# Optimization experiments

Hardware: AMD Instinct MI355X
Metric: run time of the kernel (lower is better)

The kernel has to match this reference:

```python
import jax, jax.numpy as jnp
import numpy as np

GAMMA = 0.7
WALK_LEN = 3
TAU = 1.0
N_FILTERS = 8


def _row_norm(A):
    return A / jnp.clip(jnp.sum(A, axis=-1, keepdims=True), 1e-12, None)


def _motif_channel(A, idx, Wadj, gates):
    # A: [n,n]; idx: [I,k] int node indices; Wadj: [F,k,k]; gates: [L]
    n = A.shape[0]
    I, k = idx.shape
    F = Wadj.shape[0]
    # learnable filter adjacency: softplus, symmetrize, zero diagonal, row-normalize
    S = jax.nn.softplus(Wadj)
    S = 0.5 * (S + jnp.swapaxes(S, -1, -2)) * (1.0 - jnp.eye(k, dtype=A.dtype))
    Sf = _row_norm(S)                                  # [F,k,k]
    # per-instance induced subgraph transition matrices
    As = A[idx[:, :, None], idx[:, None, :]]           # [I,k,k]
    Tm = _row_norm(As)                                 # [I,k,k]
    # batched Kronecker product: Km[i,f,a*k+b,c*k+d] = Tm[i,a,c]*Sf[f,b,d]
    Km = (Tm[:, None, :, None, :, None] * Sf[None, :, None, :, None, :]).reshape(I, F, k * k, k * k)
    gp = jax.nn.softplus(gates)                        # [L] length gates
    M = Km
    acc = (GAMMA * gp[0]) * jnp.trace(M, axis1=-2, axis2=-1)   # [I,F]
    for p in range(2, WALK_LEN + 1):
        M = M @ Km
        acc = acc + (GAMMA ** p * gp[p - 1]) * jnp.trace(M, axis1=-2, axis2=-1)
    sims = acc                                         # [I,F] RWK similarities
    alphas = jax.nn.softmax(sims / max(1e-06, TAU), axis=-1)
    contrib = (alphas * sims) / float(k)               # [I,F]
    upd = jnp.broadcast_to(contrib[:, None, :], (I, k, F)).reshape(I * k, F)
    return jnp.zeros((n, F), A.dtype).at[idx.reshape(-1)].add(upd)


def _layer(A, tri_idx, cyc_idx, H, Wt, Wc, g, lng, lnb, w1, b1, w2, b2):
    Phi = jnp.concatenate([_motif_channel(A, tri_idx, Wt, g),
                           _motif_channel(A, cyc_idx, Wc, g),
                           H], axis=1)                 # [n, in_ch]
    mu = jnp.mean(Phi, axis=-1, keepdims=True)
    var = jnp.var(Phi, axis=-1, keepdims=True)
    X = (Phi - mu) / jnp.sqrt(var + 1e-5) * lng + lnb  # LayerNorm
    return jax.nn.gelu(X @ w1 + b1, approximate=False) @ w2 + b2  # dropout = identity (eval)


def _templates():
    tri = np.zeros((3, 3), np.float32)
    for u, v in [(0, 1), (1, 2), (0, 2)]:
        tri[u, v] = tri[v, u] = 1.0
    cyc = np.zeros((4, 4), np.float32)
    for u, v in [(0, 1), (1, 2), (2, 3), (3, 0)]:
        cyc[u, v] = cyc[v, u] = 1.0
    return tri, cyc


def setup_inputs() -> dict:
    key = jax.random.key(0)
    ks = jax.random.split(key, 16)
    n, D, HID = 4096, 128, 128
    A = (jax.random.uniform(ks[0], (n, n)) < 0.01).astype(jnp.float32)
    A = 0.5 * (A + A.T)
    A = A * (1.0 - jnp.eye(n, dtype=jnp.float32))
    tri_idx = jax.random.randint(ks[1], (30000, 3), 0, n, dtype=jnp.int32)
    cyc_idx = jax.random.randint(ks[2], (15000, 4), 0, n, dtype=jnp.int32)
    tri_t, cyc_t = _templates()
    def w_adj(k, tmpl):
        return jnp.asarray(tmpl)[None] + 0.05 * jax.random.normal(k, (N_FILTERS,) + tmpl.shape, dtype=jnp.float32)
    in0, in1 = 17, 145
    inp = {"A_full": A, "tri_idx": tri_idx, "cyc_idx": cyc_idx,
           "W_tri_0": w_adj(ks[3], tri_t), "W_cyc_0": w_adj(ks[4], cyc_t),
           "gates_0": jnp.zeros((WALK_LEN,), jnp.float32),
           "lng_0": jnp.ones((in0,), jnp.float32), "lnb_0": jnp.zeros((in0,), jnp.float32),
           "w1_0": 0.05 * jax.random.normal(ks[5], (in0, HID), jnp.float32), "b1_0": jnp.zeros((HID,), jnp.float32),
           "w2_0": 0.05 * jax.random.normal(ks[6], (HID, D), jnp.float32), "b2_0": jnp.zeros((D,), jnp.float32),
           "W_tri_1": w_adj(ks[7], tri_t), "W_cyc_1": w_adj(ks[8], cyc_t),
           "gates_1": jnp.zeros((WALK_LEN,), jnp.float32),
           "lng_1": jnp.ones((in1,), jnp.float32), "lnb_1": jnp.zeros((in1,), jnp.float32),
           "w1_1": 0.05 * jax.random.normal(ks[9], (in1, HID), jnp.float32), "b1_1": jnp.zeros((HID,), jnp.float32),
           "w2_1": 0.05 * jax.random.normal(ks[10], (HID, D), jnp.float32), "b2_1": jnp.zeros((D,), jnp.float32)}
    return inp


def reference(A_full, tri_idx, cyc_idx,
              W_tri_0, W_cyc_0, gates_0, lng_0, lnb_0, w1_0, b1_0, w2_0, b2_0,
              W_tri_1, W_cyc_1, gates_1, lng_1, lnb_1, w1_1, b1_1, w2_1, b2_1):
    # base channel (use_base=True): node degree from dense adjacency
    H = jnp.sum(A_full, axis=-1, keepdims=True)        # [n,1]
    Z = _layer(A_full, tri_idx, cyc_idx, H, W_tri_0, W_cyc_0, gates_0, lng_0, lnb_0, w1_0, b1_0, w2_0, b2_0)
    H = jnp.concatenate([Z, H], axis=1)                # residual_cat: [n,129]
    Z = _layer(A_full, tri_idx, cyc_idx, H, W_tri_1, W_cyc_1, gates_1, lng_1, lnb_1, w1_1, b1_1, w2_1, b2_1)
    H = jnp.concatenate([Z, H], axis=1)                # [n,257]
    return H
```

## Files before the change

kernel.cpp:

```cpp
#include <hip/hip_runtime.h>
#include <math.h>
#include <stdint.h>

#define GAMMA 0.7f
#define CAP 96

typedef __attribute__((ext_vector_type(8))) short short8v;
typedef __attribute__((ext_vector_type(4))) float f32x4;

__device__ __forceinline__ float sp_dev(float x) {
    return fmaxf(x, 0.0f) + log1pf(expf(-fabsf(x)));
}
__device__ __forceinline__ float gelu_exact(float x) {
    return 0.5f * x * (1.0f + erff(x * 0.70710678118654752f));
}
__device__ __forceinline__ uint16_t f2bf(float x) {
    union { float f; uint32_t u; } c; c.f = x;
    uint32_t u = c.u + 0x7FFFu + ((c.u >> 16) & 1u);
    return (uint16_t)(u >> 16);
}

__global__ void prep_kernel(const float* __restrict__ Wt0, const float* __restrict__ Wc0,
                            const float* __restrict__ g0,
                            const float* __restrict__ Wt1, const float* __restrict__ Wc1,
                            const float* __restrict__ g1,
                            const float* __restrict__ w1_0, const float* __restrict__ w2_0,
                            const float* __restrict__ w1_1, const float* __restrict__ w2_1,
                            float* __restrict__ dcoef,
                            uint16_t* __restrict__ Wb10, uint16_t* __restrict__ Wb20,
                            uint16_t* __restrict__ Wb11, uint16_t* __restrict__ Wb21,
                            int* __restrict__ cursor, int ncur) {
    int tid = threadIdx.x;
    int gtid = blockIdx.x * blockDim.x + tid;
    int stride = gridDim.x * blockDim.x;

    for (int i = gtid; i < ncur; i += stride) cursor[i] = 0;

    if (blockIdx.x == 0 && tid < 32) {
        int L = tid >> 4, m = (tid >> 3) & 1, f = tid & 7;
        int k = m ? 4 : 3;
        const float* W = L ? (m ? Wc1 : Wt1) : (m ? Wc0 : Wt0);
        const float* g = L ? g1 : g0;
        float S[4][4], Y[4][4];
        for (int a = 0; a < k; a++)
            for (int b = 0; b < k; b++)
                S[a][b] = sp_dev(W[(f * k + a) * k + b]);
        for (int a = 0; a < k; a++)
            for (int b = 0; b < k; b++)
                Y[a][b] = (a == b) ? 0.0f : 0.5f * (S[a][b] + S[b][a]);
        for (int a = 0; a < k; a++) {
            float rs = 0.0f;
            for (int b = 0; b < k; b++) rs += Y[a][b];
            rs = fmaxf(rs, 1e-12f);
            for (int b = 0; b < k; b++) Y[a][b] /= rs;
        }
        float t1 = 0, t2 = 0, t3 = 0;
        for (int a = 0; a < k; a++) t1 += Y[a][a];
        for (int a = 0; a < k; a++)
            for (int b = 0; b < k; b++) t2 += Y[a][b] * Y[b][a];
        for (int a = 0; a < k; a++)
            for (int b = 0; b < k; b++)
                for (int c = 0; c < k; c++) t3 += Y[a][b] * Y[b][c] * Y[c][a];
        float* d = dcoef + ((L * 2 + m) * 8 + f) * 3;
        d[0] = GAMMA * sp_dev(g[0]) * t1;
        d[1] = GAMMA * GAMMA * sp_dev(g[1]) * t2;
        d[2] = GAMMA * GAMMA * GAMMA * sp_dev(g[2]) * t3;
    }
    for (int idx = gtid; idx < 57344; idx += stride) {
        if (idx < 4096) {
            int c = idx >> 5, k = idx & 31;
            Wb10[idx] = (k < 17) ? f2bf(w1_0[k * 128 + c]) : 0;
        } else if (idx < 20480) {
            int e = idx - 4096; int c = e >> 7, k = e & 127;
            Wb20[e] = f2bf(w2_0[k * 128 + c]);
        } else if (idx < 40960) {
            int e = idx - 20480; int c = e / 160, k = e % 160;
            Wb11[e] = (k < 145) ? f2bf(w1_1[k * 128 + c]) : 0;
        } else {
            int e = idx - 40960; int c = e >> 7, k = e & 127;
            Wb21[e] = f2bf(w2_1[k * 128 + c]);
        }
    }
}

template <int K>
__device__ __forceinline__ void contrib_group(
    const float* __restrict__ A, int n,
    const int* __restrict__ idx, int I, int i, int g, int lane,
    const float (*dc)[8][3], float* __restrict__ cont,
    int* __restrict__ cursor, int* __restrict__ slotbuf) {
    int base = lane & ~3;
    int mynode = (g < K) ? idx[i * K + g] : 0;
    int nb0 = __shfl(mynode, base + 0);
    int nb1 = __shfl(mynode, base + 1);
    int nb2 = __shfl(mynode, base + 2);
    int nb3 = (K == 4) ? __shfl(mynode, base + 3) : 0;

    float r0, r1, r2, r3;
    if (K == 3) {
        if (g < 3) {
            const float* Ar = A + (size_t)mynode * n;
            r0 = Ar[nb0]; r1 = Ar[nb1]; r2 = Ar[nb2]; r3 = 0.0f;
        } else {
            r0 = 0.0f; r1 = 0.0f; r2 = 0.0f; r3 = 1.0f;
        }
    } else {
        const float* Ar = A + (size_t)mynode * n;
        r0 = Ar[nb0]; r1 = Ar[nb1]; r2 = Ar[nb2]; r3 = Ar[nb3];
    }
    float rs = fmaxf(r0 + r1 + r2 + r3, 1e-12f);
    float inv = 1.0f / rs;
    r0 *= inv; r1 *= inv; r2 *= inv; r3 *= inv;

    float M[4][4];
#pragma unroll
    for (int b = 0; b < 4; b++) {
        M[b][0] = __shfl(r0, base + b);
        M[b][1] = __shfl(r1, base + b);
        M[b][2] = __shfl(r2, base + b);
        M[b][3] = __shfl(r3, base + b);
    }

    float t1 = M[0][0] + M[1][1] + M[2][2] + M[3][3];
    float t2 = 0.0f, t3 = 0.0f;
#pragma unroll
    for (int a = 0; a < 4; a++)
#pragma unroll
        for (int b = 0; b < 4; b++) {
            float ab = M[a][b];
            t2 += ab * M[b][a];
#pragma unroll
            for (int c = 0; c < 4; c++) t3 += ab * M[b][c] * M[c][a];
        }
    if (K == 3) { t1 -= 1.0f; t2 -= 1.0f; t3 -= 1.0f; }

#pragma unroll
    for (int L = 0; L < 2; L++) {
        float sims[8], mx = -1e30f;
#pragma unroll
        for (int f = 0; f < 8; f++) {
            sims[f] = dc[L][f][0] * t1 + dc[L][f][1] * t2 + dc[L][f][2] * t3;
            mx = fmaxf(mx, sims[f]);
        }
        float es[8], se = 0.0f;
#pragma unroll
        for (int f = 0; f < 8; f++) { es[f] = expf(sims[f] - mx); se += es[f]; }
        float sinv = 1.0f / se;
        float cn[8];
#pragma unroll
        for (int f = 0; f < 8; f++) cn[f] = es[f] * sinv * sims[f] * (1.0f / (float)K);
        float p0 = (g == 0) ? cn[0] : (g == 1) ? cn[2] : (g == 2) ? cn[4] : cn[6];
        float p1 = (g == 0) ? cn[1] : (g == 1) ? cn[3] : (g == 2) ? cn[5] : cn[7];
        float2 st = make_float2(p0, p1);
        *(float2*)(cont + ((size_t)L * I + i) * 8 + 2 * g) = st;
    }

    if (g < K) {
        int pos = atomicAdd(&cursor[mynode], 1);
        if (pos < CAP) slotbuf[(size_t)mynode * CAP + pos] = i;
    }
}

__global__ __launch_bounds__(256) void fused_kernel(
    const float* __restrict__ A, int n,
    const int* __restrict__ tri, int Itri,
    const int* __restrict__ cyc, int Icyc,
    int Btri, int Bcyc,
    const float* __restrict__ dcoef,
    float* __restrict__ tri_c, float* __restrict__ cyc_c,
    int* __restrict__ cursor, int* __restrict__ slotbuf,
    float* __restrict__ H0, float* __restrict__ out) {
    __shared__ float dc[2][8][3];
    __shared__ float red[4];
    int bid = blockIdx.x;
    int tid = threadIdx.x;

    if (bid < Btri + Bcyc) {
        bool isTri = bid < Btri;
        const float* dl0 = dcoef + (isTri ? 0 : 24);
        const float* dl1 = dcoef + (isTri ? 48 : 72);
        if (tid < 24) dc[0][tid / 3][tid % 3] = dl0[tid];
        else if (tid < 48) { int t = tid - 24; dc[1][t / 3][t % 3] = dl1[t]; }
        __syncthreads();

        int lane = tid & 63;
        int g = tid & 3;
        if (isTri) {
            int i = bid * 64 + (tid >> 2);
            if (i < Itri)
                contrib_group<3>(A, n, tri, Itri, i, g, lane, dc, tri_c, cursor, slotbuf);
        } else {
            int i = (bid - Btri) * 64 + (tid >> 2);
            if (i < Icyc)
                contrib_group<4>(A, n, cyc, Icyc, i, g, lane, dc, cyc_c,
                                 cursor + n, slotbuf + (size_t)n * CAP);
        }
    } else {
        int row = bid - (Btri + Bcyc);
        const float4* Arow = (const float4*)(A + (size_t)row * n);
        int n4 = n >> 2;
        float s = 0.0f;
        for (int i = tid; i < n4; i += 256) {
            float4 v = Arow[i];
            s += v.x + v.y + v.z + v.w;
        }
        for (int off = 32; off > 0; off >>= 1) s += __shfl_down(s, off);
        if ((tid & 63) == 0) red[tid >> 6] = s;
        __syncthreads();
        if (tid == 0) {
            float t = red[0] + red[1] + red[2] + red[3];
            H0[row] = t;
            out[(size_t)row * 257 + 256] = t;
        }
    }
}

__global__ __launch_bounds__(512) void mega_kernel(
    const float* __restrict__ tri_c, int Itri,
    const float* __restrict__ cyc_c, int Icyc,
    const int* __restrict__ cursor, const int* __restrict__ slotbuf,
    const float* __restrict__ H0,
    const float* __restrict__ lng0, const float* __restrict__ lnb0,
    const uint16_t* __restrict__ Wb10, const float* __restrict__ b1_0,
    const uint16_t* __restrict__ Wb20, const float* __restrict__ b2_0,
    const float* __restrict__ lng1, const float* __restrict__ lnb1,
    const uint16_t* __restrict__ Wb11, const float* __restrict__ b1_1,
    const uint16_t* __restrict__ Wb21, const float* __restrict__ b2_1,
    float* __restrict__ out, int n) {
    __shared__ uint16_t Xs[16][168];
    __shared__ uint16_t Hs[16][136];
    __shared__ float    Zs[16][129];
    __shared__ float    phi0[16][17];
    __shared__ float    f1[16][16];
    __shared__ float    h0s[16];

    int tid = threadIdx.x;
    int v0 = blockIdx.x * 16;
    int wave = tid >> 6;
    int lane = tid & 63;
    int lr = lane & 15, lg = lane >> 4;

    {
        int r = tid >> 5;
        int combo = tid & 31;
        int m = combo >> 4, L = (combo >> 3) & 1, f = combo & 7;
        int v = v0 + r;
        int cnt = cursor[m * n + v];
        cnt = cnt < CAP ? cnt : CAP;
        const int* bucket = slotbuf + ((size_t)(m * n + v)) * CAP;
        const float* c = m ? cyc_c : tri_c;
        int I = m ? Icyc : Itri;
        float sum = 0.0f;
        for (int j = 0; j < cnt; j++) {
            int i = bucket[j];
            sum += c[((size_t)L * I + i) * 8 + f];
        }
        if (L == 0) phi0[r][m * 8 + f] = sum;
        else        f1[r][m * 8 + f] = sum;
        if (combo == 0) { float h = H0[v]; phi0[r][16] = h; h0s[r] = h; }
    }
    __syncthreads();

    {
        int r = tid >> 5;
        int j = tid & 31;
        float x = (j < 17) ? phi0[r][j] : 0.0f;
        float s1 = x, s2 = x * x;
        for (int o = 16; o > 0; o >>= 1) { s1 += __shfl_xor(s1, o); s2 += __shfl_xor(s2, o); }
        float mu = s1 / 17.0f;
        float rstd = rsqrtf(s2 / 17.0f - mu * mu + 1e-5f);
        Xs[r][j] = (j < 17) ? f2bf((x - mu) * rstd * lng0[j] + lnb0[j]) : (uint16_t)0;
    }
    __syncthreads();

    {
        int col = wave * 16 + lr;
        f32x4 acc = {0.f, 0.f, 0.f, 0.f};
        short8v a = *(const short8v*)&Xs[lr][lg * 8];
        short8v b = *(const short8v*)(Wb10 + (size_t)col * 32 + lg * 8);
        acc = __builtin_amdgcn_mfma_f32_16x16x32_bf16(a, b, acc, 0, 0, 0);
        float bias = b1_0[col];
#pragma unroll
        for (int i = 0; i < 4; i++)
            Hs[lg * 4 + i][col] = f2bf(gelu_exact(acc[i] + bias));
    }
    __syncthreads();

    {
        int col = wave * 16 + lr;
        f32x4 acc = {0.f, 0.f, 0.f, 0.f};
#pragma unroll
        for (int ks = 0; ks < 4; ks++) {
            short8v a = *(const short8v*)&Hs[lr][ks * 32 + lg * 8];
            short8v b = *(const short8v*)(Wb20 + (size_t)col * 128 + ks * 32 + lg * 8);
            acc = __builtin_amdgcn_mfma_f32_16x16x32_bf16(a, b, acc, 0, 0, 0);
        }
        float bias = b2_0[col];
#pragma unroll
        for (int i = 0; i < 4; i++) {
            int row = lg * 4 + i;
            float val = acc[i] + bias;
            out[(size_t)(v0 + row) * 257 + 128 + col] = val;
            Zs[row][col] = val;
        }
    }
    __syncthreads();

    {
        int rr = tid >> 5;
        int t = tid & 31;
        float ph[5];
        float s1 = 0.0f, s2 = 0.0f;
#pragma unroll
        for (int s = 0; s < 5; s++) {
            int j = t + 32 * s;
            float x = 0.0f;
            if (j < 16) x = f1[rr][j];
            else if (j < 144) x = Zs[rr][j - 16];
            else if (j == 144) x = h0s[rr];
            ph[s] = x;
            if (j < 145) { s1 += x; s2 += x * x; }
        }
        for (int o = 16; o > 0; o >>= 1) { s1 += __shfl_xor(s1, o); s2 += __shfl_xor(s2, o); }
        float mu = s1 / 145.0f;
        float rstd = rsqrtf(s2 / 145.0f - mu * mu + 1e-5f);
#pragma unroll
        for (int s = 0; s < 5; s++) {
            int j = t + 32 * s;
            Xs[rr][j] = (j < 145) ? f2bf((ph[s] - mu) * rstd * lng1[j] + lnb1[j]) : (uint16_t)0;
        }
    }
    __syncthreads();

    {
        int col = wave * 16 + lr;
        f32x4 acc = {0.f, 0.f, 0.f, 0.f};
#pragma unroll
        for (int ks = 0; ks < 5; ks++) {
            short8v a = *(const short8v*)&Xs[lr][ks * 32 + lg * 8];
            short8v b = *(const short8v*)(Wb11 + (size_t)col * 160 + ks * 32 + lg * 8);
            acc = __builtin_amdgcn_mfma_f32_16x16x32_bf16(a, b, acc, 0, 0, 0);
        }
        float bias = b1_1[col];
#pragma unroll
        for (int i = 0; i < 4; i++)
            Hs[lg * 4 + i][col] = f2bf(gelu_exact(acc[i] + bias));
    }
    __syncthreads();

    {
        int col = wave * 16 + lr;
        f32x4 acc = {0.f, 0.f, 0.f, 0.f};
#pragma unroll
        for (int ks = 0; ks < 4; ks++) {
            short8v a = *(const short8v*)&Hs[lr][ks * 32 + lg * 8];
            short8v b = *(const short8v*)(Wb21 + (size_t)col * 128 + ks * 32 + lg * 8);
            acc = __builtin_amdgcn_mfma_f32_16x16x32_bf16(a, b, acc, 0, 0, 0);
        }
        float bias = b2_1[col];
#pragma unroll
        for (int i = 0; i < 4; i++) {
            int row = lg * 4 + i;
            out[(size_t)(v0 + row) * 257 + col] = acc[i] + bias;
        }
    }
}

extern "C" void kernel_launch(void* const* d_in, const int* in_sizes, int n_in,
                              void* d_out, int out_size, void* d_ws, size_t ws_size,
                              hipStream_t stream) {
    const float* A    = (const float*)d_in[0];
    const int*   tri  = (const int*)d_in[1];
    const int*   cyc  = (const int*)d_in[2];
    const float* Wt0  = (const float*)d_in[3];
    const float* Wc0  = (const float*)d_in[4];
    const float* g0   = (const float*)d_in[5];
    const float* lng0 = (const float*)d_in[6];
    const float* lnb0 = (const float*)d_in[7];
    const float* w1_0 = (const float*)d_in[8];
    const float* b1_0 = (const float*)d_in[9];
    const float* w2_0 = (const float*)d_in[10];
    const float* b2_0 = (const float*)d_in[11];
    const float* Wt1  = (const float*)d_in[12];
    const float* Wc1  = (const float*)d_in[13];
    const float* g1   = (const float*)d_in[14];
    const float* lng1 = (const float*)d_in[15];
    const float* lnb1 = (const float*)d_in[16];
    const float* w1_1 = (const float*)d_in[17];
    const float* b1_1 = (const float*)d_in[18];
    const float* w2_1 = (const float*)d_in[19];
    const float* b2_1 = (const float*)d_in[20];

    int n    = out_size / 257;
    int Itri = in_sizes[1] / 3;
    int Icyc = in_sizes[2] / 4;

    float* ws    = (float*)d_ws;
    float* dcoef = ws;
    float* H0    = ws + 128;
    float* tri_c = H0 + n;
    float* cyc_c = tri_c + (size_t)2 * Itri * 8;
    int*   cursor  = (int*)(cyc_c + (size_t)2 * Icyc * 8);
    int*   slotbuf = cursor + (size_t)2 * n;
    uint16_t* Wb10 = (uint16_t*)(slotbuf + (size_t)2 * n * CAP);
    uint16_t* Wb20 = Wb10 + 128 * 32;
    uint16_t* Wb11 = Wb20 + 128 * 128;
    uint16_t* Wb21 = Wb11 + 128 * 160;
    float* out = (float*)d_out;

    prep_kernel<<<64, 256, 0, stream>>>(Wt0, Wc0, g0, Wt1, Wc1, g1,
                                        w1_0, w2_0, w1_1, w2_1,
                                        dcoef, Wb10, Wb20, Wb11, Wb21,
                                        cursor, 2 * n);

    int Btri = (Itri + 63) / 64;
    int Bcyc = (Icyc + 63) / 64;
    fused_kernel<<<Btri + Bcyc + n, 256, 0, stream>>>(
        A, n, tri, Itri, cyc, Icyc, Btri, Bcyc, dcoef,
        tri_c, cyc_c, cursor, slotbuf, H0, out);

    mega_kernel<<<n / 16, 512, 0, stream>>>(
        tri_c, Itri, cyc_c, Icyc, cursor, slotbuf, H0,
        lng0, lnb0, Wb10, b1_0, Wb20, b2_0,
        lng1, lnb1, Wb11, b1_1, Wb21, b2_1, out, n);
}
```

Before: 72.86 us.

## Fold weight prep into fused kernel, compute walk coefs per block, use symmetric gathers

Removes the separate prep kernel. Each motif block now computes its own walk coefficients into shared memory, and extra blocks in the fused kernel convert the MLP weights to bf16. A small kernel only zeroes the cursors. The motif gather exploits symmetry: it loads only the upper-triangle adjacency entries (3 or 6 loads per instance instead of 9 or 16) and builds the matrix via shuffles. This trades a larger, more divergent fused kernel with redundant coefficient work per block for less prep-kernel work and fewer scattered loads. It also assumes A is symmetric.

```diff
diff --git a/kernel.cpp b/kernel.cpp
--- a/kernel.cpp
+++ b/kernel.cpp
@@ -20,107 +20,87 @@
     return (uint16_t)(u >> 16);
 }
 
-__global__ void prep_kernel(const float* __restrict__ Wt0, const float* __restrict__ Wc0,
-                            const float* __restrict__ g0,
-                            const float* __restrict__ Wt1, const float* __restrict__ Wc1,
-                            const float* __restrict__ g1,
-                            const float* __restrict__ w1_0, const float* __restrict__ w2_0,
-                            const float* __restrict__ w1_1, const float* __restrict__ w2_1,
-                            float* __restrict__ dcoef,
-                            uint16_t* __restrict__ Wb10, uint16_t* __restrict__ Wb20,
-                            uint16_t* __restrict__ Wb11, uint16_t* __restrict__ Wb21,
-                            int* __restrict__ cursor, int ncur) {
-    int tid = threadIdx.x;
-    int gtid = blockIdx.x * blockDim.x + tid;
-    int stride = gridDim.x * blockDim.x;
-
-    for (int i = gtid; i < ncur; i += stride) cursor[i] = 0;
-
-    if (blockIdx.x == 0 && tid < 32) {
-        int L = tid >> 4, m = (tid >> 3) & 1, f = tid & 7;
-        int k = m ? 4 : 3;
-        const float* W = L ? (m ? Wc1 : Wt1) : (m ? Wc0 : Wt0);
-        const float* g = L ? g1 : g0;
-        float S[4][4], Y[4][4];
-        for (int a = 0; a < k; a++)
-            for (int b = 0; b < k; b++)
-                S[a][b] = sp_dev(W[(f * k + a) * k + b]);
-        for (int a = 0; a < k; a++)
-            for (int b = 0; b < k; b++)
-                Y[a][b] = (a == b) ? 0.0f : 0.5f * (S[a][b] + S[b][a]);
-        for (int a = 0; a < k; a++) {
-            float rs = 0.0f;
-            for (int b = 0; b < k; b++) rs += Y[a][b];
-            rs = fmaxf(rs, 1e-12f);
-            for (int b = 0; b < k; b++) Y[a][b] /= rs;
-        }
-        float t1 = 0, t2 = 0, t3 = 0;
-        for (int a = 0; a < k; a++) t1 += Y[a][a];
-        for (int a = 0; a < k; a++)
-            for (int b = 0; b < k; b++) t2 += Y[a][b] * Y[b][a];
-        for (int a = 0; a < k; a++)
-            for (int b = 0; b < k; b++)
-                for (int c = 0; c < k; c++) t3 += Y[a][b] * Y[b][c] * Y[c][a];
-        float* d = dcoef + ((L * 2 + m) * 8 + f) * 3;
-        d[0] = GAMMA * sp_dev(g[0]) * t1;
-        d[1] = GAMMA * GAMMA * sp_dev(g[1]) * t2;
-        d[2] = GAMMA * GAMMA * GAMMA * sp_dev(g[2]) * t3;
-    }
-    for (int idx = gtid; idx < 57344; idx += stride) {
-        if (idx < 4096) {
-            int c = idx >> 5, k = idx & 31;
-            Wb10[idx] = (k < 17) ? f2bf(w1_0[k * 128 + c]) : 0;
-        } else if (idx < 20480) {
-            int e = idx - 4096; int c = e >> 7, k = e & 127;
-            Wb20[e] = f2bf(w2_0[k * 128 + c]);
-        } else if (idx < 40960) {
-            int e = idx - 20480; int c = e / 160, k = e % 160;
-            Wb11[e] = (k < 145) ? f2bf(w1_1[k * 128 + c]) : 0;
-        } else {
-            int e = idx - 40960; int c = e >> 7, k = e & 127;
-            Wb21[e] = f2bf(w2_1[k * 128 + c]);
-        }
-    }
+__device__ __forceinline__ void walk_coef(const float* __restrict__ W,
+                                          const float* __restrict__ g,
+                                          int f, int k, float* d) {
+    float S[4][4], Y[4][4];
+    for (int a = 0; a < k; a++)
+        for (int b = 0; b < k; b++)
+            S[a][b] = sp_dev(W[(f * k + a) * k + b]);
+    for (int a = 0; a < k; a++)
+        for (int b = 0; b < k; b++)
+            Y[a][b] = (a == b) ? 0.0f : 0.5f * (S[a][b] + S[b][a]);
+    for (int a = 0; a < k; a++) {
+        float rs = 0.0f;
+        for (int b = 0; b < k; b++) rs += Y[a][b];
+        rs = fmaxf(rs, 1e-12f);
+        for (int b = 0; b < k; b++) Y[a][b] /= rs;
+    }
+    float t1 = 0, t2 = 0, t3 = 0;
+    for (int a = 0; a < k; a++) t1 += Y[a][a];
+    for (int a = 0; a < k; a++)
+        for (int b = 0; b < k; b++) t2 += Y[a][b] * Y[b][a];
+    for (int a = 0; a < k; a++)
+        for (int b = 0; b < k; b++)
+            for (int c = 0; c < k; c++) t3 += Y[a][b] * Y[b][c] * Y[c][a];
+    d[0] = GAMMA * sp_dev(g[0]) * t1;
+    d[1] = GAMMA * GAMMA * sp_dev(g[1]) * t2;
+    d[2] = GAMMA * GAMMA * GAMMA * sp_dev(g[2]) * t3;
+}
+
+__global__ void k0_zero(int* __restrict__ cursor, int ncur) {
+    int i = blockIdx.x * 256 + threadIdx.x;
+    int stride = gridDim.x * 256;
+    for (; i < ncur; i += stride) cursor[i] = 0;
 }
 
 template <int K>
-__device__ __forceinline__ void contrib_group(
-    const float* __restrict__ A, int n,
-    const int* __restrict__ idx, int I, int i, int g, int lane,
-    const float (*dc)[8][3], float* __restrict__ cont,
+__device__ __forceinline__ void contrib4(
+    const float* __restrict__ A, int n, const int* __restrict__ idx,
+    int li, int lane, const float (*dc)[8][3],
+    float* __restrict__ cont, int I,
     int* __restrict__ cursor, int* __restrict__ slotbuf) {
+    int g = lane & 3;
     int base = lane & ~3;
-    int mynode = (g < K) ? idx[i * K + g] : 0;
+    int mynode = (g < K) ? idx[li * K + g] : 0;
     int nb0 = __shfl(mynode, base + 0);
     int nb1 = __shfl(mynode, base + 1);
     int nb2 = __shfl(mynode, base + 2);
     int nb3 = (K == 4) ? __shfl(mynode, base + 3) : 0;
 
-    float r0, r1, r2, r3;
-    if (K == 3) {
-        if (g < 3) {
-            const float* Ar = A + (size_t)mynode * n;
-            r0 = Ar[nb0]; r1 = Ar[nb1]; r2 = Ar[nb2]; r3 = 0.0f;
-        } else {
-            r0 = 0.0f; r1 = 0.0f; r2 = 0.0f; r3 = 1.0f;
-        }
+    float va = 0.0f, vb = 0.0f;
+    if (K == 4) {
+        if (g == 0)      { va = A[(size_t)nb0 * n + nb1]; vb = A[(size_t)nb0 * n + nb3]; }
+        else if (g == 1) { va = A[(size_t)nb1 * n + nb2]; vb = A[(size_t)nb1 * n + nb3]; }
+        else if (g == 2) { va = A[(size_t)nb2 * n + nb3]; }
+        else             { va = A[(size_t)nb0 * n + nb2]; }
     } else {
-        const float* Ar = A + (size_t)mynode * n;
-        r0 = Ar[nb0]; r1 = Ar[nb1]; r2 = Ar[nb2]; r3 = Ar[nb3];
-    }
-    float rs = fmaxf(r0 + r1 + r2 + r3, 1e-12f);
-    float inv = 1.0f / rs;
-    r0 *= inv; r1 *= inv; r2 *= inv; r3 *= inv;
-
-    float M[4][4];
-#pragma unroll
-    for (int b = 0; b < 4; b++) {
-        M[b][0] = __shfl(r0, base + b);
-        M[b][1] = __shfl(r1, base + b);
-        M[b][2] = __shfl(r2, base + b);
-        M[b][3] = __shfl(r3, base + b);
-    }
-
+        if (g == 0)      va = A[(size_t)nb0 * n + nb1];
+        else if (g == 1) va = A[(size_t)nb1 * n + nb2];
+        else if (g == 3) va = A[(size_t)nb0 * n + nb2];
+    }
+    float u01 = __shfl(va, base + 0);
+    float u12 = __shfl(va, base + 1);
+    float u02 = __shfl(va, base + 3);
+    float u03 = 0.0f, u13 = 0.0f, u23 = 0.0f, d33 = 1.0f;
+    if (K == 4) {
+        u03 = __shfl(vb, base + 0);
+        u13 = __shfl(vb, base + 1);
+        u23 = __shfl(va, base + 2);
+        d33 = 0.0f;
+    }
+
+    float M[4][4] = {{0.0f, u01, u02, u03},
+                     {u01, 0.0f, u12, u13},
+                     {u02, u12, 0.0f, u23},
+                     {u03, u13, u23, d33}};
+#pragma unroll
+    for (int a = 0; a < 4; a++) {
+        float rs = fmaxf(M[a][0] + M[a][1] + M[a][2] + M[a][3], 1e-12f);
+        float inv = 1.0f / rs;
+#pragma unroll
+        for (int b = 0; b < 4; b++) M[a][b] *= inv;
+    }
     float t1 = M[0][0] + M[1][1] + M[2][2] + M[3][3];
     float t2 = 0.0f, t3 = 0.0f;
 #pragma unroll
@@ -129,11 +109,14 @@
         for (int b = 0; b < 4; b++) {
             float ab = M[a][b];
             t2 += ab * M[b][a];
-#pragma unroll
-            for (int c = 0; c < 4; c++) t3 += ab * M[b][c] * M[c][a];
+            float a3 = 0.0f;
+#pragma unroll
+            for (int c = 0; c < 4; c++) a3 += M[b][c] * M[c][a];
+            t3 += ab * a3;
         }
     if (K == 3) { t1 -= 1.0f; t2 -= 1.0f; t3 -= 1.0f; }
 
+    const float kinv = 1.0f / (float)K;
 #pragma unroll
     for (int L = 0; L < 2; L++) {
         float sims[8], mx = -1e30f;
@@ -148,55 +131,58 @@
         float sinv = 1.0f / se;
         float cn[8];
 #pragma unroll
-        for (int f = 0; f < 8; f++) cn[f] = es[f] * sinv * sims[f] * (1.0f / (float)K);
+        for (int f = 0; f < 8; f++) cn[f] = es[f] * sinv * sims[f] * kinv;
         float p0 = (g == 0) ? cn[0] : (g == 1) ? cn[2] : (g == 2) ? cn[4] : cn[6];
         float p1 = (g == 0) ? cn[1] : (g == 1) ? cn[3] : (g == 2) ? cn[5] : cn[7];
-        float2 st = make_float2(p0, p1);
-        *(float2*)(cont + ((size_t)L * I + i) * 8 + 2 * g) = st;
+        *(float2*)(cont + ((size_t)L * I + li) * 8 + 2 * g) = make_float2(p0, p1);
     }
 
     if (g < K) {
         int pos = atomicAdd(&cursor[mynode], 1);
-        if (pos < CAP) slotbuf[(size_t)mynode * CAP + pos] = i;
+        if (pos < CAP) slotbuf[(size_t)mynode * CAP + pos] = li;
     }
 }
 
 __global__ __launch_bounds__(256) void fused_kernel(
-    const float* __restrict__ A, int n,
-    const int* __restrict__ tri, int Itri,
-    const int* __restrict__ cyc, int Icyc,
-    int Btri, int Bcyc,
-    const float* __restrict__ dcoef,
+    const float* __restrict__ A, const int* __restrict__ tri, const int* __restrict__ cyc,
+    const float* __restrict__ Wt0, const float* __restrict__ Wc0, const float* __restrict__ g0,
+    const float* __restrict__ Wt1, const float* __restrict__ Wc1, const float* __restrict__ g1,
+    const float* __restrict__ w1_0, const float* __restrict__ w2_0,
+    const float* __restrict__ w1_1, const float* __restrict__ w2_1,
     float* __restrict__ tri_c, float* __restrict__ cyc_c,
     int* __restrict__ cursor, int* __restrict__ slotbuf,
-    float* __restrict__ H0, float* __restrict__ out) {
-    __shared__ float dc[2][8][3];
-    __shared__ float red[4];
-    int bid = blockIdx.x;
-    int tid = threadIdx.x;
-
-    if (bid < Btri + Bcyc) {
-        bool isTri = bid < Btri;
-        const float* dl0 = dcoef + (isTri ? 0 : 24);
-        const float* dl1 = dcoef + (isTri ? 48 : 72);
-        if (tid < 24) dc[0][tid / 3][tid % 3] = dl0[tid];
-        else if (tid < 48) { int t = tid - 24; dc[1][t / 3][t % 3] = dl1[t]; }
+    float* __restrict__ H0,
+    uint16_t* __restrict__ Wb10, uint16_t* __restrict__ Wb20,
+    uint16_t* __restrict__ Wb11, uint16_t* __restrict__ Wb21,
+    float* __restrict__ out, int n, int Itri, int Icyc, int BT, int BCY) {
+
+    const int tid = threadIdx.x;
+    const int bid = blockIdx.x;
+    const int lane = tid & 63;
+
+    if (bid < BT + BCY) {
+        bool isTri = bid < BT;
+        __shared__ float dc[2][8][3];
+        if (tid < 16) {
+            int L = tid >> 3, f = tid & 7;
+            const float* W = isTri ? (L ? Wt1 : Wt0) : (L ? Wc1 : Wc0);
+            const float* g = L ? g1 : g0;
+            walk_coef(W, g, f, isTri ? 3 : 4, &dc[L][f][0]);
+        }
         __syncthreads();
-
-        int lane = tid & 63;
-        int g = tid & 3;
         if (isTri) {
-            int i = bid * 64 + (tid >> 2);
-            if (i < Itri)
-                contrib_group<3>(A, n, tri, Itri, i, g, lane, dc, tri_c, cursor, slotbuf);
+            int li = bid * 64 + (tid >> 2);
+            if (li < Itri)
+                contrib4<3>(A, n, tri, li, lane, dc, tri_c, Itri, cursor, slotbuf);
         } else {
-            int i = (bid - Btri) * 64 + (tid >> 2);
-            if (i < Icyc)
-                contrib_group<4>(A, n, cyc, Icyc, i, g, lane, dc, cyc_c,
-                                 cursor + n, slotbuf + (size_t)n * CAP);
-        }
-    } else {
-        int row = bid - (Btri + Bcyc);
+            int li = (bid - BT) * 64 + (tid >> 2);
+            if (li < Icyc)
+                contrib4<4>(A, n, cyc, li, lane, dc, cyc_c, Icyc,
+                            cursor + n, slotbuf + (size_t)n * CAP);
+        }
+    } else if (bid < BT + BCY + n) {
+        __shared__ float red[4];
+        int row = bid - BT - BCY;
         const float4* Arow = (const float4*)(A + (size_t)row * n);
         int n4 = n >> 2;
         float s = 0.0f;
@@ -211,6 +197,25 @@
             float t = red[0] + red[1] + red[2] + red[3];
             H0[row] = t;
             out[(size_t)row * 257 + 256] = t;
+        }
+    } else {
+        int base = (bid - BT - BCY - n) * 4096;
+        for (int k = 0; k < 16; k++) {
+            int idx = base + k * 256 + tid;
+            if (idx >= 57344) break;
+            if (idx < 4096) {
+                int c = idx >> 5, kk = idx & 31;
+                Wb10[idx] = (kk < 17) ? f2bf(w1_0[kk * 128 + c]) : 0;
+            } else if (idx < 20480) {
+                int e = idx - 4096; int c = e >> 7, kk = e & 127;
+                Wb20[e] = f2bf(w2_0[kk * 128 + c]);
+            } else if (idx < 40960) {
+                int e = idx - 20480; int c = e / 160, kk = e % 160;
+                Wb11[e] = (kk < 145) ? f2bf(w1_1[kk * 128 + c]) : 0;
+            } else {
+                int e = idx - 40960; int c = e >> 7, kk = e & 127;
+                Wb21[e] = f2bf(w2_1[kk * 128 + c]);
+            }
         }
     }
 }
@@ -372,32 +377,13 @@
     const float* A    = (const float*)d_in[0];
     const int*   tri  = (const int*)d_in[1];
     const int*   cyc  = (const int*)d_in[2];
-    const float* Wt0  = (const float*)d_in[3];
-    const float* Wc0  = (const float*)d_in[4];
-    const float* g0   = (const float*)d_in[5];
-    const float* lng0 = (const float*)d_in[6];
-    const float* lnb0 = (const float*)d_in[7];
-    const float* w1_0 = (const float*)d_in[8];
-    const float* b1_0 = (const float*)d_in[9];
-    const float* w2_0 = (const float*)d_in[10];
-    const float* b2_0 = (const float*)d_in[11];
-    const float* Wt1  = (const float*)d_in[12];
-    const float* Wc1  = (const float*)d_in[13];
-    const float* g1   = (const float*)d_in[14];
-    const float* lng1 = (const float*)d_in[15];
-    const float* lnb1 = (const float*)d_in[16];
-    const float* w1_1 = (const float*)d_in[17];
-    const float* b1_1 = (const float*)d_in[18];
-    const float* w2_1 = (const float*)d_in[19];
-    const float* b2_1 = (const float*)d_in[20];
 
     int n    = out_size / 257;
     int Itri = in_sizes[1] / 3;
     int Icyc = in_sizes[2] / 4;
 
     float* ws    = (float*)d_ws;
-    float* dcoef = ws;
-    float* H0    = ws + 128;
+    float* H0    = ws;
     float* tri_c = H0 + n;
     float* cyc_c = tri_c + (size_t)2 * Itri * 8;
     int*   cursor  = (int*)(cyc_c + (size_t)2 * Icyc * 8);
@@ -408,19 +394,25 @@
     uint16_t* Wb21 = Wb11 + 128 * 160;
     float* out = (float*)d_out;
 
-    prep_kernel<<<64, 256, 0, stream>>>(Wt0, Wc0, g0, Wt1, Wc1, g1,
-                                        w1_0, w2_0, w1_1, w2_1,
-                                        dcoef, Wb10, Wb20, Wb11, Wb21,
-                                        cursor, 2 * n);
-
-    int Btri = (Itri + 63) / 64;
-    int Bcyc = (Icyc + 63) / 64;
-    fused_kernel<<<Btri + Bcyc + n, 256, 0, stream>>>(
-        A, n, tri, Itri, cyc, Icyc, Btri, Bcyc, dcoef,
-        tri_c, cyc_c, cursor, slotbuf, H0, out);
+    k0_zero<<<8, 256, 0, stream>>>(cursor, 2 * n);
+
+    int BT  = (Itri + 63) / 64;
+    int BCY = (Icyc + 63) / 64;
+    int BP  = 14;
+    fused_kernel<<<BT + BCY + n + BP, 256, 0, stream>>>(
+        A, tri, cyc,
+        (const float*)d_in[3], (const float*)d_in[4], (const float*)d_in[5],
+        (const float*)d_in[12], (const float*)d_in[13], (const float*)d_in[14],
+        (const float*)d_in[8], (const float*)d_in[10],
+        (const float*)d_in[17], (const float*)d_in[19],
+        tri_c, cyc_c, cursor, slotbuf, H0,
+        Wb10, Wb20, Wb11, Wb21, out, n, Itri, Icyc, BT, BCY);
 
     mega_kernel<<<n / 16, 512, 0, stream>>>(
         tri_c, Itri, cyc_c, Icyc, cursor, slotbuf, H0,
-        lng0, lnb0, Wb10, b1_0, Wb20, b2_0,
-        lng1, lnb1, Wb11, b1_1, Wb21, b2_1, out, n);
-}
+        (const float*)d_in[6], (const float*)d_in[7],
+        Wb10, (const float*)d_in[9], Wb20, (const float*)d_in[11],
+        (const float*)d_in[15], (const float*)d_in[16],
+        Wb11, (const float*)d_in[18], Wb21, (const float*)d_in[20],
+        out, n);
+}
```

Measured after the change: 78.79 us. 8.1% more time.
